# Performance work log

Measured on AMD Instinct MI355X. Metric: run time of the kernel, lower is better.

Reference implementation:

```python
import jax, jax.numpy as jnp
import numpy as np

N_NODES = 50000
E_HALF = 500000
N_FEAT = 5
GCN_DIMS = [32, 64, 128]
MLP_DIMS = [128, 64]


def _lin_init(key, fan_in, fan_out):
    return jax.random.normal(key, (fan_in, fan_out), dtype=jnp.float32) / np.sqrt(fan_in)


def setup_inputs() -> dict:
    key = jax.random.key(0)
    ks = jax.random.split(key, 20)
    x = jax.random.normal(ks[0], (N_NODES, N_FEAT), dtype=jnp.float32)
    src = jax.random.randint(ks[1], (E_HALF,), 0, N_NODES)
    dst = jax.random.randint(ks[2], (E_HALF,), 0, N_NODES)
    # paired edges: second half is the reversed direction of the first half
    edges = jnp.stack([jnp.concatenate([src, dst]), jnp.concatenate([dst, src])], axis=0).astype(jnp.int64)
    edge_attr = jax.random.uniform(ks[3], (2 * E_HALF, 2), dtype=jnp.float32)
    detector_labels = jnp.ones((N_NODES,), dtype=bool)
    inp = {"x": x, "edges": edges, "edge_attr": edge_attr, "detector_labels": detector_labels}
    # GraphConv params: out = agg @ w_rel + x @ w_root + b
    dims = [N_FEAT] + GCN_DIMS
    for i, (di, do) in enumerate(zip(dims[:-1], dims[1:])):
        inp[f"w_rel{i}"] = _lin_init(ks[4 + 3 * i], di, do)
        inp[f"w_root{i}"] = _lin_init(ks[5 + 3 * i], di, do)
        inp[f"b{i}"] = jnp.zeros((do,), dtype=jnp.float32)
    # edge MLP: transition_dim = 2*128 + 1 = 257
    mdims = [2 * GCN_DIMS[-1] + 1] + MLP_DIMS
    for i, (di, do) in enumerate(zip(mdims[:-1], mdims[1:])):
        inp[f"w_d{i}"] = _lin_init(ks[13 + 2 * i], di, do)
        inp[f"b_d{i}"] = jnp.zeros((do,), dtype=jnp.float32)
    inp["w_out"] = _lin_init(ks[17], MLP_DIMS[-1], 1)
    inp["b_out"] = jnp.zeros((1,), dtype=jnp.float32)
    return inp


def reference(x, edges, edge_attr, detector_labels,
              w_rel0, w_root0, b0, w_rel1, w_root1, b1, w_rel2, w_root2, b2,
              w_d0, b_d0, w_d1, b_d1, w_out, b_out):
    n = x.shape[0]
    src, dst = edges[0], edges[1]
    w = edge_attr[:, 0] * edge_attr[:, 1]  # [E]

    def gconv(h, wr, wro, b):
        msg = h[src] * w[:, None]                                   # gather + scale  [E, d]
        agg = jax.ops.segment_sum(msg, dst, num_segments=n)          # scatter-add     [N, d]
        return jnp.tanh(agg @ wr + h @ wro + b)

    h = gconv(x, w_rel0, w_root0, b0)
    h = gconv(h, w_rel1, w_root1, b1)
    h = gconv(h, w_rel2, w_root2, b2)

    # SplitSyndromes: keep edges whose both endpoints are detector nodes
    # (indices are concrete, so this is computed with numpy -> static shapes)
    e_np = np.asarray(edges)
    subset = np.arange(n)[np.asarray(detector_labels)]
    valid = np.isin(e_np, subset).sum(axis=0) == 2
    keep = np.nonzero(valid)[0]
    edges_f = jnp.asarray(e_np[:, keep])
    ea = edge_attr[keep]

    ef = jnp.concatenate([h[edges_f[0]], ea[:, :1], h[edges_f[1]]], axis=-1)  # [Ef, 257]
    ef = jnp.tanh(ef @ w_d0 + b_d0)
    ef = jnp.tanh(ef @ w_d1 + b_d1)
    ef = ef @ w_out + b_out                                                   # [Ef, 1]

    half = ef.shape[0] // 2
    ef2 = ef.reshape(2, half)
    classes = ea[:, 1].reshape(2, half)
    mi = jnp.argmin(ef2, axis=0)                                              # [half]
    ef_sel = jnp.take_along_axis(ef2, mi[None, :], axis=0)[0]
    cls_sel = jnp.take_along_axis(classes, mi[None, :], axis=0)[0]
    return edges_f[:, :half], ef_sel, cls_sel
```

## Files before the change

### kernel.cpp

```cpp
#include <hip/hip_runtime.h>
#include <hip/hip_bf16.h>


typedef __attribute__((ext_vector_type(8))) short short8;
typedef __attribute__((ext_vector_type(4))) float f32x4;

__device__ __forceinline__ float fast_tanh(float x) {
    float e = __expf(2.0f * x);
    return 1.0f - 2.0f * __builtin_amdgcn_rcpf(e + 1.0f);
}
__device__ __forceinline__ float b2f(unsigned short u) {
    union { unsigned i; float f; } c; c.i = ((unsigned)u) << 16; return c.f;
}
__device__ __forceinline__ short f2b(float f) {
    __hip_bfloat16 h = __float2bfloat16(f);
    return *reinterpret_cast<short*>(&h);
}
__device__ __forceinline__ float ldf(float v) { return v; }
__device__ __forceinline__ float ldf(unsigned short v) { return b2f(v); }


__global__ void deg_count(const int* __restrict__ ed, int* __restrict__ deg, int E) {
    int e = blockIdx.x * blockDim.x + threadIdx.x;
    if (e < E) atomicAdd(&deg[ed[E + e]], 1);
}

__global__ __launch_bounds__(1024) void scan_build(const int* __restrict__ deg,
                                                   int* __restrict__ off, int* __restrict__ cur,
                                                   int n) {
    __shared__ int part[1024];
    const int tid = threadIdx.x;
    const int chunk = (n + 1023) >> 10;
    const int b = tid * chunk;
    int s = 0;
    for (int i = 0; i < chunk; ++i) {
        int j = b + i;
        if (j < n) s += deg[j];
    }
    part[tid] = s;
    __syncthreads();
    for (int d = 1; d < 1024; d <<= 1) {
        int v = (tid >= d) ? part[tid - d] : 0;
        __syncthreads();
        part[tid] += v;
        __syncthreads();
    }
    int run = tid ? part[tid - 1] : 0;
    for (int i = 0; i < chunk; ++i) {
        int j = b + i;
        if (j < n) {
            off[j] = run;
            cur[j] = run;
            run += deg[j];
        }
    }
    if (tid == 1023) off[n] = run;
}

__global__ void csr_fill(const int* __restrict__ ed, const float* __restrict__ ea,
                         int* __restrict__ cur, int* __restrict__ srcl,
                         float* __restrict__ wl, int* __restrict__ posl,
                         float* __restrict__ eal, int E) {
    int e = blockIdx.x * blockDim.x + threadIdx.x;
    if (e >= E) return;
    int d = ed[E + e];
    int pos = atomicAdd(&cur[d], 1);
    srcl[pos] = ed[e];
    wl[pos] = ea[2 * e] * ea[2 * e + 1];
    eal[pos] = ea[2 * e];
    posl[e] = pos;
}


__global__ void gather_agg5(const float* __restrict__ x, const int* __restrict__ off,
                            const int* __restrict__ srcl, const float* __restrict__ wl,
                            float* __restrict__ agg, int n) {
    int idx = blockIdx.x * blockDim.x + threadIdx.x;
    int node = idx >> 3;
    int q = idx & 7;
    if (node >= n || q >= 5) return;
    int b = off[node], en = off[node + 1];
    float acc = 0.f;
    int j = b;
    for (; j + 2 <= en; j += 2) {
        int s0 = srcl[j], s1 = srcl[j + 1];
        float w0 = wl[j], w1 = wl[j + 1];
        acc += x[(size_t)s0 * 5 + q] * w0 + x[(size_t)s1 * 5 + q] * w1;
    }
    if (j < en) acc += x[(size_t)srcl[j] * 5 + q] * wl[j];
    agg[(size_t)node * 5 + q] = acc;
}

template <int D>
__global__ void gather_agg_b(const unsigned short* __restrict__ h, const int* __restrict__ off,
                             const int* __restrict__ srcl, const float* __restrict__ wl,
                             float* __restrict__ agg, int n) {
    constexpr int TPN = D / 8;
    int idx = blockIdx.x * blockDim.x + threadIdx.x;
    int node = idx / TPN;
    int q = idx % TPN;
    if (node >= n) return;
    int b = off[node], en = off[node + 1];
    float acc[8] = {0, 0, 0, 0, 0, 0, 0, 0};
    int j = b;
#pragma unroll 1
    for (; j + 2 <= en; j += 2) {
        int s0 = srcl[j], s1 = srcl[j + 1];
        float w0 = wl[j], w1 = wl[j + 1];
        short8 v0 = *(const short8*)&h[(size_t)s0 * D + q * 8];
        short8 v1 = *(const short8*)&h[(size_t)s1 * D + q * 8];
#pragma unroll
        for (int m = 0; m < 8; ++m)
            acc[m] += b2f((unsigned short)v0[m]) * w0 + b2f((unsigned short)v1[m]) * w1;
    }
    if (j < en) {
        int s = srcl[j];
        float w = wl[j];
        short8 v = *(const short8*)&h[(size_t)s * D + q * 8];
#pragma unroll
        for (int m = 0; m < 8; ++m) acc[m] += b2f((unsigned short)v[m]) * w;
    }
    float4* ag = (float4*)&agg[(size_t)node * D + q * 8];
    ag[0] = make_float4(acc[0], acc[1], acc[2], acc[3]);
    ag[1] = make_float4(acc[4], acc[5], acc[6], acc[7]);
}


template <int DIN, int DOUT, typename TI>
__global__ void node_update_b(const TI* __restrict__ hin, const float* __restrict__ agg,
                              const float* __restrict__ wrel, const float* __restrict__ wroot,
                              const float* __restrict__ bias, unsigned short* __restrict__ hout,
                              int n) {
    int idx = blockIdx.x * blockDim.x + threadIdx.x;
    if (idx >= n * DOUT) return;
    int node = idx / DOUT;
    int c = idx - node * DOUT;
    const float* ag = agg + (size_t)node * DIN;
    const TI* hi = hin + (size_t)node * DIN;
    float acc = bias[c];
#pragma unroll
    for (int k = 0; k < DIN; ++k)
        acc += ag[k] * wrel[k * DOUT + c] + ldf(hi[k]) * wroot[k * DOUT + c];
    hout[idx] = (unsigned short)f2b(fast_tanh(acc));
}


__global__ void prep_weights(const float* __restrict__ wd0, const float* __restrict__ wd1,
                             unsigned short* __restrict__ w0t, unsigned short* __restrict__ w1t) {
    int idx = blockIdx.x * blockDim.x + threadIdx.x;
    if (idx < 128 * 256) {
        int c = idx >> 8, k = idx & 255;
        int kr = (k < 128) ? k : k + 1;
        w0t[idx] = (unsigned short)f2b(wd0[(size_t)kr * 128 + c]);
    } else {
        int j = idx - 128 * 256;
        if (j < 64 * 128) {
            int c = j >> 7, k = j & 127;
            w1t[j] = (unsigned short)f2b(wd1[(size_t)k * 64 + c]);
        }
    }
}


__global__ __launch_bounds__(256) void uv_gemm(
    const unsigned short* __restrict__ h3b, const unsigned short* __restrict__ w0t,
    const float* __restrict__ bd0,
    unsigned short* __restrict__ Ub, unsigned short* __restrict__ Vb, int n) {
    __shared__ __align__(16) unsigned short A[64 * 152];

    const int tid = threadIdx.x;
    const int wid = tid >> 6;
    const int lane = tid & 63;
    const int l15 = lane & 15;
    const int g = lane >> 4;
    const int base = blockIdx.x * 64;

#pragma unroll
    for (int i = 0; i < 4; ++i) {
        int cid = i * 256 + tid;
        int row = cid >> 4;
        int c8 = cid & 15;
        int node = base + row;
        if (node >= n) node = n - 1;
        *(short8*)&A[row * 152 + c8 * 8] = *(const short8*)&h3b[(size_t)node * 128 + c8 * 8];
    }

    const int koff = (wid < 2) ? 0 : 128;
    short8 bf[4][4];
#pragma unroll
    for (int ct = 0; ct < 4; ++ct) {
        int c = ((wid & 1) * 64 + 16 * ct + l15);
#pragma unroll
        for (int ks = 0; ks < 4; ++ks)
            bf[ct][ks] = *(const short8*)&w0t[(size_t)c * 256 + koff + ks * 32 + g * 8];
    }
    __syncthreads();

    f32x4 acc[4][4];
#pragma unroll
    for (int rt = 0; rt < 4; ++rt)
#pragma unroll
        for (int ct = 0; ct < 4; ++ct) acc[rt][ct] = (f32x4){0.f, 0.f, 0.f, 0.f};

#pragma unroll
    for (int rt = 0; rt < 4; ++rt) {
        short8 af[4];
#pragma unroll
        for (int ks = 0; ks < 4; ++ks)
            af[ks] = *(const short8*)&A[(16 * rt + l15) * 152 + ks * 32 + g * 8];
#pragma unroll
        for (int ct = 0; ct < 4; ++ct)
#pragma unroll
            for (int ks = 0; ks < 4; ++ks)
                acc[rt][ct] = __builtin_amdgcn_mfma_f32_16x16x32_bf16(af[ks], bf[ct][ks],
                                                                     acc[rt][ct], 0, 0, 0);
    }

    unsigned short* outp = (wid < 2) ? Ub : Vb;
    const int cb = (wid & 1) * 64;
    float b0v[4];
#pragma unroll
    for (int ct = 0; ct < 4; ++ct)
        b0v[ct] = (wid < 2) ? 0.f : bd0[cb + 16 * ct + l15];
#pragma unroll
    for (int rt = 0; rt < 4; ++rt)
#pragma unroll
        for (int ct = 0; ct < 4; ++ct) {
            int c = cb + 16 * ct + l15;
#pragma unroll
            for (int j = 0; j < 4; ++j) {
                int node = base + 16 * rt + 4 * g + j;
                if (node < n)
                    outp[(size_t)node * 128 + c] = (unsigned short)f2b(acc[rt][ct][j] + b0v[ct]);
            }
        }
}


__global__ __launch_bounds__(256) void edge_mlp_uv(
    const unsigned short* __restrict__ Ub, const unsigned short* __restrict__ Vb,
    const int* __restrict__ srcl, const int* __restrict__ off,
    int n, const float* __restrict__ eal, const unsigned short* __restrict__ w1t,
    const float* __restrict__ wd0,
    const float* __restrict__ bd1, const float* __restrict__ wout,
    const float* __restrict__ bout, float* __restrict__ ef, int E) {
    __shared__ int SRC[64], DST[64];
    __shared__ float EAs[64], WEA[128], B1[64], WOUT[64];

    const int tid = threadIdx.x;
    const int wid = tid >> 6;
    const int lane = tid & 63;
    const int l15 = lane & 15;
    const int g = lane >> 4;
    const int geb = blockIdx.x * 64;

    if (tid < 64) {
        int p = geb + tid;
        SRC[tid] = srcl[p];
        EAs[tid] = eal[p];
        int lo = 0, hi = n;
        while (hi - lo > 1) {
            int mid = (lo + hi) >> 1;
            if (off[mid] <= p) lo = mid; else hi = mid;
        }
        DST[tid] = lo;
    } else if (tid < 192) {
        int c = tid - 64;
        WEA[c] = wd0[(size_t)128 * 128 + c];
    } else {
        int c = tid - 192;
        B1[c] = bd1[c];
        WOUT[c] = wout[c];
    }
    __syncthreads();

    short8 bf[4][4];
#pragma unroll
    for (int ct = 0; ct < 4; ++ct)
#pragma unroll
        for (int ks = 0; ks < 4; ++ks)
            bf[ct][ks] = *(const short8*)&w1t[(size_t)(16 * ct + l15) * 128 + ks * 32 + g * 8];

    const int r = 16 * wid + l15;
    const int src = SRC[r], dst = DST[r];
    const float eav = EAs[r];

    short8 u[4], v[4];
#pragma unroll
    for (int ks = 0; ks < 4; ++ks) {
        u[ks] = *(const short8*)&Ub[(size_t)src * 128 + ks * 32 + g * 8];
        v[ks] = *(const short8*)&Vb[(size_t)dst * 128 + ks * 32 + g * 8];
    }

    f32x4 acc1[4];
#pragma unroll
    for (int ct = 0; ct < 4; ++ct) acc1[ct] = (f32x4){0.f, 0.f, 0.f, 0.f};

#pragma unroll
    for (int ks = 0; ks < 4; ++ks) {
        short8 af;
#pragma unroll
        for (int m = 0; m < 8; ++m) {
            int kk = ks * 32 + g * 8 + m;
            float o = b2f((unsigned short)u[ks][m]) + b2f((unsigned short)v[ks][m]) + eav * WEA[kk];
            af[m] = f2b(fast_tanh(o));
        }
#pragma unroll
        for (int ct = 0; ct < 4; ++ct)
            acc1[ct] = __builtin_amdgcn_mfma_f32_16x16x32_bf16(af, bf[ct][ks], acc1[ct], 0, 0, 0);
    }

    float p4[4] = {0.f, 0.f, 0.f, 0.f};
#pragma unroll
    for (int ct = 0; ct < 4; ++ct) {
        int col = 16 * ct + l15;
        float b1v = B1[col], wo = WOUT[col];
#pragma unroll
        for (int j = 0; j < 4; ++j) p4[j] += fast_tanh(acc1[ct][j] + b1v) * wo;
    }
#pragma unroll
    for (int j = 0; j < 4; ++j) {
        p4[j] += __shfl_xor(p4[j], 1);
        p4[j] += __shfl_xor(p4[j], 2);
        p4[j] += __shfl_xor(p4[j], 4);
        p4[j] += __shfl_xor(p4[j], 8);
    }
    if (l15 == 0) {
        float bo = bout[0];
#pragma unroll
        for (int j = 0; j < 4; ++j) ef[geb + 16 * wid + 4 * g + j] = p4[j] + bo;
    }
}


__global__ void finalize(const int* __restrict__ ed, const float* __restrict__ ea,
                         const float* __restrict__ ef, const int* __restrict__ posl,
                         float* __restrict__ out, int half, int E) {
    int i = blockIdx.x * blockDim.x + threadIdx.x;
    if (i >= half) return;
    float f0 = ef[posl[i]];
    float f1 = ef[posl[i + half]];
    int mi = (f1 < f0) ? 1 : 0;
    float fs = mi ? f1 : f0;
    float cs = ea[2 * (i + mi * half) + 1];
    out[i] = (float)ed[i];
    out[half + i] = (float)ed[E + i];
    out[2 * half + i] = fs;
    out[3 * half + i] = cs;
}


extern "C" void kernel_launch(void* const* d_in, const int* in_sizes, int n_in,
                              void* d_out, int out_size, void* d_ws, size_t ws_size,
                              hipStream_t stream) {
    const float* x = (const float*)d_in[0];
    const int* edges = (const int*)d_in[1];
    const float* ea = (const float*)d_in[2];
    const float* w_rel0 = (const float*)d_in[4];
    const float* w_root0 = (const float*)d_in[5];
    const float* b0 = (const float*)d_in[6];
    const float* w_rel1 = (const float*)d_in[7];
    const float* w_root1 = (const float*)d_in[8];
    const float* b1 = (const float*)d_in[9];
    const float* w_rel2 = (const float*)d_in[10];
    const float* w_root2 = (const float*)d_in[11];
    const float* b2 = (const float*)d_in[12];
    const float* w_d0 = (const float*)d_in[13];
    const float* b_d0 = (const float*)d_in[14];
    const float* w_d1 = (const float*)d_in[15];
    const float* b_d1 = (const float*)d_in[16];
    const float* w_out = (const float*)d_in[17];
    const float* b_out = (const float*)d_in[18];

    const int n = in_sizes[0] / 5;
    const int E = in_sizes[2] / 2;
    const int half = E / 2;

    float* ws = (float*)d_ws;
    size_t o_srcl = (size_t)n * 64;
    size_t o_posl = o_srcl + E;
    size_t o_off  = o_posl + E;
    size_t o_cur  = o_off + 51000;
    size_t o_deg  = o_cur + 50000;
    size_t o_eal  = o_deg + 50000;
    size_t o_w0t  = o_eal + E;
    size_t o_w1t  = o_w0t + 16384;

    unsigned short* h1b = (unsigned short*)ws;
    unsigned short* h3b = (unsigned short*)ws;
    float* ef = ws;
    int* srcl = (int*)(ws + o_srcl);
    int* posl = (int*)(ws + o_posl);
    int* off = (int*)(ws + o_off);
    int* cur = (int*)(ws + o_cur);
    int* deg = (int*)(ws + o_deg);
    float* eal = ws + o_eal;
    unsigned short* w0t = (unsigned short*)(ws + o_w0t);
    unsigned short* w1t = (unsigned short*)(ws + o_w1t);
    unsigned short* h2b = (unsigned short*)(ws + (size_t)n * 128);
    float* wl = ws + (size_t)n * 160;
    unsigned short* Ub = (unsigned short*)(ws + (size_t)n * 128);
    float* agg = ws + (size_t)n * 192;
    unsigned short* Vb = (unsigned short*)(ws + (size_t)n * 192);

    float* out = (float*)d_out;
    const int B = 256;

    hipMemsetAsync(deg, 0, (size_t)n * sizeof(int), stream);
    deg_count<<<(E + B - 1) / B, B, 0, stream>>>(edges, deg, E);
    scan_build<<<1, 1024, 0, stream>>>(deg, off, cur, n);
    csr_fill<<<(E + B - 1) / B, B, 0, stream>>>(edges, ea, cur, srcl, wl, posl, eal, E);

    gather_agg5<<<((size_t)n * 8 + B - 1) / B, B, 0, stream>>>(x, off, srcl, wl, agg, n);
    node_update_b<5, 32, float><<<(n * 32 + B - 1) / B, B, 0, stream>>>(
        x, agg, w_rel0, w_root0, b0, h1b, n);

    gather_agg_b<32><<<((size_t)n * 4 + B - 1) / B, B, 0, stream>>>(h1b, off, srcl, wl, agg, n);
    node_update_b<32, 64, unsigned short><<<(n * 64 + B - 1) / B, B, 0, stream>>>(
        h1b, agg, w_rel1, w_root1, b1, h2b, n);

    gather_agg_b<64><<<((size_t)n * 8 + B - 1) / B, B, 0, stream>>>(h2b, off, srcl, wl, agg, n);
    node_update_b<64, 128, unsigned short><<<(n * 128 + B - 1) / B, B, 0, stream>>>(
        h2b, agg, w_rel2, w_root2, b2, h3b, n);

    prep_weights<<<160, B, 0, stream>>>(w_d0, w_d1, w0t, w1t);
    uv_gemm<<<(n + 63) / 64, B, 0, stream>>>(h3b, w0t, b_d0, Ub, Vb, n);
    edge_mlp_uv<<<E / 64, B, 0, stream>>>(Ub, Vb, srcl, off, n, eal, w1t,
                                          w_d0, b_d1, w_out, b_out, ef, E);

    finalize<<<(half + B - 1) / B, B, 0, stream>>>(edges, ea, ef, posl, out, half, E);
}
```

Baseline: 794.9 us.

## Pack CSR edge records, reuse atomic ranks, store aggregates in bf16

The degree-count atomics now record each edge's rank, so the CSR fill computes its slot as off+rank and no longer needs a second pass of atomics or a cursor array. Source index and weight are packed into one int2 record, and edge_attr and the original edge id go into a second int2. The MLP writes ef directly at the original edge index, which removes the posl indirection in finalize. Gather loops unroll by four, and aggregates are stored as bf16 to cut write and read traffic, at some cost in accuracy. The workspace is reorganised around fixed hardcoded offsets.

```diff
diff --git a/kernel.cpp b/kernel.cpp
--- a/kernel.cpp
+++ b/kernel.cpp
@@ -20,14 +20,14 @@
 __device__ __forceinline__ float ldf(unsigned short v) { return b2f(v); }
 
 
-__global__ void deg_count(const int* __restrict__ ed, int* __restrict__ deg, int E) {
+__global__ void deg_count(const int* __restrict__ ed, int* __restrict__ deg,
+                          int* __restrict__ rank, int E) {
     int e = blockIdx.x * blockDim.x + threadIdx.x;
-    if (e < E) atomicAdd(&deg[ed[E + e]], 1);
+    if (e < E) rank[e] = atomicAdd(&deg[ed[E + e]], 1);
 }
 
 __global__ __launch_bounds__(1024) void scan_build(const int* __restrict__ deg,
-                                                   int* __restrict__ off, int* __restrict__ cur,
-                                                   int n) {
+                                                   int* __restrict__ off, int n) {
     __shared__ int part[1024];
     const int tid = threadIdx.x;
     const int chunk = (n + 1023) >> 10;
@@ -50,7 +50,6 @@
         int j = b + i;
         if (j < n) {
             off[j] = run;
-            cur[j] = run;
             run += deg[j];
         }
     }
@@ -58,23 +57,22 @@
 }
 
 __global__ void csr_fill(const int* __restrict__ ed, const float* __restrict__ ea,
-                         int* __restrict__ cur, int* __restrict__ srcl,
-                         float* __restrict__ wl, int* __restrict__ posl,
-                         float* __restrict__ eal, int E) {
+                         const int* __restrict__ off, const int* __restrict__ rank,
+                         int2* __restrict__ recA, int2* __restrict__ recB, int E) {
     int e = blockIdx.x * blockDim.x + threadIdx.x;
     if (e >= E) return;
     int d = ed[E + e];
-    int pos = atomicAdd(&cur[d], 1);
-    srcl[pos] = ed[e];
-    wl[pos] = ea[2 * e] * ea[2 * e + 1];
-    eal[pos] = ea[2 * e];
-    posl[e] = pos;
+    int pos = off[d] + rank[e];
+    float ea0 = ea[2 * e];
+    float w = ea0 * ea[2 * e + 1];
+    recA[pos] = make_int2(ed[e], __float_as_int(w));
+    recB[pos] = make_int2(__float_as_int(ea0), e);
 }
 
 
 __global__ void gather_agg5(const float* __restrict__ x, const int* __restrict__ off,
-                            const int* __restrict__ srcl, const float* __restrict__ wl,
-                            float* __restrict__ agg, int n) {
+                            const int2* __restrict__ recA, unsigned short* __restrict__ agg,
+                            int n) {
     int idx = blockIdx.x * blockDim.x + threadIdx.x;
     int node = idx >> 3;
     int q = idx & 7;
@@ -82,19 +80,24 @@
     int b = off[node], en = off[node + 1];
     float acc = 0.f;
     int j = b;
-    for (; j + 2 <= en; j += 2) {
-        int s0 = srcl[j], s1 = srcl[j + 1];
-        float w0 = wl[j], w1 = wl[j + 1];
-        acc += x[(size_t)s0 * 5 + q] * w0 + x[(size_t)s1 * 5 + q] * w1;
-    }
-    if (j < en) acc += x[(size_t)srcl[j] * 5 + q] * wl[j];
-    agg[(size_t)node * 5 + q] = acc;
+    for (; j + 4 <= en; j += 4) {
+        int2 r0 = recA[j], r1 = recA[j + 1], r2 = recA[j + 2], r3 = recA[j + 3];
+        acc += x[(size_t)r0.x * 5 + q] * __int_as_float(r0.y) +
+               x[(size_t)r1.x * 5 + q] * __int_as_float(r1.y) +
+               x[(size_t)r2.x * 5 + q] * __int_as_float(r2.y) +
+               x[(size_t)r3.x * 5 + q] * __int_as_float(r3.y);
+    }
+    for (; j < en; ++j) {
+        int2 r = recA[j];
+        acc += x[(size_t)r.x * 5 + q] * __int_as_float(r.y);
+    }
+    agg[(size_t)node * 5 + q] = (unsigned short)f2b(acc);
 }
 
 template <int D>
 __global__ void gather_agg_b(const unsigned short* __restrict__ h, const int* __restrict__ off,
-                             const int* __restrict__ srcl, const float* __restrict__ wl,
-                             float* __restrict__ agg, int n) {
+                             const int2* __restrict__ recA, unsigned short* __restrict__ agg,
+                             int n) {
     constexpr int TPN = D / 8;
     int idx = blockIdx.x * blockDim.x + threadIdx.x;
     int node = idx / TPN;
@@ -104,30 +107,36 @@
     float acc[8] = {0, 0, 0, 0, 0, 0, 0, 0};
     int j = b;
 #pragma unroll 1
-    for (; j + 2 <= en; j += 2) {
-        int s0 = srcl[j], s1 = srcl[j + 1];
-        float w0 = wl[j], w1 = wl[j + 1];
-        short8 v0 = *(const short8*)&h[(size_t)s0 * D + q * 8];
-        short8 v1 = *(const short8*)&h[(size_t)s1 * D + q * 8];
+    for (; j + 4 <= en; j += 4) {
+        int2 r0 = recA[j], r1 = recA[j + 1], r2 = recA[j + 2], r3 = recA[j + 3];
+        short8 v0 = *(const short8*)&h[(size_t)r0.x * D + q * 8];
+        short8 v1 = *(const short8*)&h[(size_t)r1.x * D + q * 8];
+        short8 v2 = *(const short8*)&h[(size_t)r2.x * D + q * 8];
+        short8 v3 = *(const short8*)&h[(size_t)r3.x * D + q * 8];
+        float w0 = __int_as_float(r0.y), w1 = __int_as_float(r1.y);
+        float w2 = __int_as_float(r2.y), w3 = __int_as_float(r3.y);
 #pragma unroll
         for (int m = 0; m < 8; ++m)
-            acc[m] += b2f((unsigned short)v0[m]) * w0 + b2f((unsigned short)v1[m]) * w1;
-    }
-    if (j < en) {
-        int s = srcl[j];
-        float w = wl[j];
-        short8 v = *(const short8*)&h[(size_t)s * D + q * 8];
+            acc[m] += b2f((unsigned short)v0[m]) * w0 + b2f((unsigned short)v1[m]) * w1 +
+                      b2f((unsigned short)v2[m]) * w2 + b2f((unsigned short)v3[m]) * w3;
+    }
+#pragma unroll 1
+    for (; j < en; ++j) {
+        int2 r = recA[j];
+        float w = __int_as_float(r.y);
+        short8 v = *(const short8*)&h[(size_t)r.x * D + q * 8];
 #pragma unroll
         for (int m = 0; m < 8; ++m) acc[m] += b2f((unsigned short)v[m]) * w;
     }
-    float4* ag = (float4*)&agg[(size_t)node * D + q * 8];
-    ag[0] = make_float4(acc[0], acc[1], acc[2], acc[3]);
-    ag[1] = make_float4(acc[4], acc[5], acc[6], acc[7]);
+    short8 o;
+#pragma unroll
+    for (int m = 0; m < 8; ++m) o[m] = f2b(acc[m]);
+    *(short8*)&agg[(size_t)node * D + q * 8] = o;
 }
 
 
 template <int DIN, int DOUT, typename TI>
-__global__ void node_update_b(const TI* __restrict__ hin, const float* __restrict__ agg,
+__global__ void node_update_b(const TI* __restrict__ hin, const unsigned short* __restrict__ agg,
                               const float* __restrict__ wrel, const float* __restrict__ wroot,
                               const float* __restrict__ bias, unsigned short* __restrict__ hout,
                               int n) {
@@ -135,12 +144,12 @@
     if (idx >= n * DOUT) return;
     int node = idx / DOUT;
     int c = idx - node * DOUT;
-    const float* ag = agg + (size_t)node * DIN;
+    const unsigned short* ag = agg + (size_t)node * DIN;
     const TI* hi = hin + (size_t)node * DIN;
     float acc = bias[c];
 #pragma unroll
     for (int k = 0; k < DIN; ++k)
-        acc += ag[k] * wrel[k * DOUT + c] + ldf(hi[k]) * wroot[k * DOUT + c];
+        acc += b2f(ag[k]) * wrel[k * DOUT + c] + ldf(hi[k]) * wroot[k * DOUT + c];
     hout[idx] = (unsigned short)f2b(fast_tanh(acc));
 }
 
@@ -239,12 +248,12 @@
 
 __global__ __launch_bounds__(256) void edge_mlp_uv(
     const unsigned short* __restrict__ Ub, const unsigned short* __restrict__ Vb,
-    const int* __restrict__ srcl, const int* __restrict__ off,
-    int n, const float* __restrict__ eal, const unsigned short* __restrict__ w1t,
+    const int2* __restrict__ recA, const int2* __restrict__ recB,
+    const int* __restrict__ off, int n, const unsigned short* __restrict__ w1t,
     const float* __restrict__ wd0,
     const float* __restrict__ bd1, const float* __restrict__ wout,
     const float* __restrict__ bout, float* __restrict__ ef, int E) {
-    __shared__ int SRC[64], DST[64];
+    __shared__ int SRC[64], DST[64], EID[64];
     __shared__ float EAs[64], WEA[128], B1[64], WOUT[64];
 
     const int tid = threadIdx.x;
@@ -256,8 +265,11 @@
 
     if (tid < 64) {
         int p = geb + tid;
-        SRC[tid] = srcl[p];
-        EAs[tid] = eal[p];
+        int2 a = recA[p];
+        int2 b = recB[p];
+        SRC[tid] = a.x;
+        EAs[tid] = __int_as_float(b.x);
+        EID[tid] = b.y;
         int lo = 0, hi = n;
         while (hi - lo > 1) {
             int mid = (lo + hi) >> 1;
@@ -328,18 +340,18 @@
     if (l15 == 0) {
         float bo = bout[0];
 #pragma unroll
-        for (int j = 0; j < 4; ++j) ef[geb + 16 * wid + 4 * g + j] = p4[j] + bo;
+        for (int j = 0; j < 4; ++j) ef[EID[16 * wid + 4 * g + j]] = p4[j] + bo;
     }
 }
 
 
 __global__ void finalize(const int* __restrict__ ed, const float* __restrict__ ea,
-                         const float* __restrict__ ef, const int* __restrict__ posl,
-                         float* __restrict__ out, int half, int E) {
+                         const float* __restrict__ ef, float* __restrict__ out,
+                         int half, int E) {
     int i = blockIdx.x * blockDim.x + threadIdx.x;
     if (i >= half) return;
-    float f0 = ef[posl[i]];
-    float f1 = ef[posl[i + half]];
+    float f0 = ef[i];
+    float f1 = ef[i + half];
     int mi = (f1 < f0) ? 1 : 0;
     float fs = mi ? f1 : f0;
     float cs = ea[2 * (i + mi * half) + 1];
@@ -377,56 +389,45 @@
     const int half = E / 2;
 
     float* ws = (float*)d_ws;
-    size_t o_srcl = (size_t)n * 64;
-    size_t o_posl = o_srcl + E;
-    size_t o_off  = o_posl + E;
-    size_t o_cur  = o_off + 51000;
-    size_t o_deg  = o_cur + 50000;
-    size_t o_eal  = o_deg + 50000;
-    size_t o_w0t  = o_eal + E;
-    size_t o_w1t  = o_w0t + 16384;
-
+    int2* recA = (int2*)(ws + 3200000);
+    int2* recB = (int2*)(ws + 5200000);
+    int* off = (int*)(ws + 7200000);
+    int* deg = (int*)(ws + 7251008);
+    unsigned short* w0t = (unsigned short*)(ws + 7301008);
+    unsigned short* w1t = (unsigned short*)(ws + 7317392);
     unsigned short* h1b = (unsigned short*)ws;
     unsigned short* h3b = (unsigned short*)ws;
-    float* ef = ws;
-    int* srcl = (int*)(ws + o_srcl);
-    int* posl = (int*)(ws + o_posl);
-    int* off = (int*)(ws + o_off);
-    int* cur = (int*)(ws + o_cur);
-    int* deg = (int*)(ws + o_deg);
-    float* eal = ws + o_eal;
-    unsigned short* w0t = (unsigned short*)(ws + o_w0t);
-    unsigned short* w1t = (unsigned short*)(ws + o_w1t);
-    unsigned short* h2b = (unsigned short*)(ws + (size_t)n * 128);
-    float* wl = ws + (size_t)n * 160;
-    unsigned short* Ub = (unsigned short*)(ws + (size_t)n * 128);
-    float* agg = ws + (size_t)n * 192;
-    unsigned short* Vb = (unsigned short*)(ws + (size_t)n * 192);
+    unsigned short* Ub = (unsigned short*)ws;
+    unsigned short* h2b = (unsigned short*)(ws + 7400000);
+    unsigned short* agg = (unsigned short*)(ws + 9000000);
+    unsigned short* Vb = (unsigned short*)(ws + 7400000);
+    float* ef = ws + 10600000;
+    int* rank = (int*)(ws + 11600000);
 
     float* out = (float*)d_out;
     const int B = 256;
 
     hipMemsetAsync(deg, 0, (size_t)n * sizeof(int), stream);
-    deg_count<<<(E + B - 1) / B, B, 0, stream>>>(edges, deg, E);
-    scan_build<<<1, 1024, 0, stream>>>(deg, off, cur, n);
-    csr_fill<<<(E + B - 1) / B, B, 0, stream>>>(edges, ea, cur, srcl, wl, posl, eal, E);
-
-    gather_agg5<<<((size_t)n * 8 + B - 1) / B, B, 0, stream>>>(x, off, srcl, wl, agg, n);
+    deg_count<<<(E + B - 1) / B, B, 0, stream>>>(edges, deg, rank, E);
+    scan_build<<<1, 1024, 0, stream>>>(deg, off, n);
+    csr_fill<<<(E + B - 1) / B, B, 0, stream>>>(edges, ea, off, rank, recA, recB, E);
+
+    gather_agg5<<<((size_t)n * 8 + B - 1) / B, B, 0, stream>>>(x, off, recA, agg, n);
     node_update_b<5, 32, float><<<(n * 32 + B - 1) / B, B, 0, stream>>>(
         x, agg, w_rel0, w_root0, b0, h1b, n);
 
-    gather_agg_b<32><<<((size_t)n * 4 + B - 1) / B, B, 0, stream>>>(h1b, off, srcl, wl, agg, n);
+    gather_agg_b<32><<<((size_t)n * 4 + B - 1) / B, B, 0, stream>>>(h1b, off, recA, agg, n);
     node_update_b<32, 64, unsigned short><<<(n * 64 + B - 1) / B, B, 0, stream>>>(
         h1b, agg, w_rel1, w_root1, b1, h2b, n);
 
-    gather_agg_b<64><<<((size_t)n * 8 + B - 1) / B, B, 0, stream>>>(h2b, off, srcl, wl, agg, n);
+    gather_agg_b<64><<<((size_t)n * 8 + B - 1) / B, B, 0, stream>>>(h2b, off, recA, agg, n);
     node_update_b<64, 128, unsigned short><<<(n * 128 + B - 1) / B, B, 0, stream>>>(
         h2b, agg, w_rel2, w_root2, b2, h3b, n);
 
     prep_weights<<<160, B, 0, stream>>>(w_d0, w_d1, w0t, w1t);
     uv_gemm<<<(n + 63) / 64, B, 0, stream>>>(h3b, w0t, b_d0, Ub, Vb, n);
-    edge_mlp_uv<<<E / 64, B, 0, stream>>>(Ub, Vb, srcl, off, n, eal, w1t,
+    edge_mlp_uv<<<E / 64, B, 0, stream>>>(Ub, Vb, recA, recB, off, n, w1t,
                                           w_d0, b_d1, w_out, b_out, ef, E);
 
-    finalize<<<(half + B - 1) / B, B, 0, stream>>>(edges, ea, ef, posl, out, half, E);
-}
+    finalize<<<(half + B - 1) / B, B, 0, stream>>>(edges, ea, ef, out, half, E);
+}
```

Result: faster. 705.8 us (-11.2%).
